# Kernel tuning notes

Hardware: AMD Instinct MI355X
Metric: run time of the kernel (lower is better)

## Reference

```python
import jax, jax.numpy as jnp
import numpy as np

N_NODES = 50000
N_EDGES = 400000
N_GRAPHS = 250
D = 256
NUM_FEATURES = 256
NUM_CLASSES = 10
N_EXTRA_LAYERS = 4  # num_layers - 1
BN_EPS = 1e-5


def _mean_agg(x, src, dst, n):
    # DGL copy_u + mean over incoming edges; zero in-degree nodes get 0.
    s = jax.ops.segment_sum(x[src], dst, num_segments=n)           # [N, d]
    deg = jax.ops.segment_sum(jnp.ones((src.shape[0],), x.dtype), dst, num_segments=n)
    deg = deg[:, None]
    return jnp.where(deg > 0, s / jnp.maximum(deg, 1.0), 0.0)


def _gin_layer(x, src, dst, W1, b1, W2, b2, gamma, beta):
    n = x.shape[0]
    h = x + _mean_agg(x, src, dst, n)                              # (1+eps)*x + agg, eps=0
    h = jax.nn.relu(h @ W1 + b1) @ W2 + b2                         # apply_func MLP
    h = jax.nn.relu(h)                                             # GINConv activation
    mu = h.mean(axis=0)
    var = h.var(axis=0)                                            # biased var (torch BN train)
    return gamma * (h - mu) / jnp.sqrt(var + BN_EPS) + beta


def setup_inputs() -> dict:
    key = jax.random.key(0)
    ks = jax.random.split(key, 24)
    sc_in = 1.0 / np.sqrt(NUM_FEATURES)
    sc = 1.0 / np.sqrt(D)
    inp = {
        "x": jax.random.normal(ks[0], (N_NODES, NUM_FEATURES), dtype=jnp.float32),
        "src": jax.random.randint(ks[1], (N_EDGES,), 0, N_NODES, dtype=jnp.int32),
        "dst": jax.random.randint(ks[2], (N_EDGES,), 0, N_NODES, dtype=jnp.int32),
        "node_counts": jnp.full((N_GRAPHS,), N_NODES // N_GRAPHS, dtype=jnp.int32),
        # conv1 MLP + BN1
        "W1a": jax.random.normal(ks[3], (NUM_FEATURES, D), dtype=jnp.float32) * sc_in,
        "b1a": jnp.zeros((D,), jnp.float32),
        "W1b": jax.random.normal(ks[4], (D, D), dtype=jnp.float32) * sc,
        "b1b": jnp.zeros((D,), jnp.float32),
        "g1": jnp.ones((D,), jnp.float32),
        "be1": jnp.zeros((D,), jnp.float32),
        # stacked convs 2..5 + BNs
        "Ws1": jax.random.normal(ks[5], (N_EXTRA_LAYERS, D, D), dtype=jnp.float32) * sc,
        "bs1": jnp.zeros((N_EXTRA_LAYERS, D), jnp.float32),
        "Ws2": jax.random.normal(ks[6], (N_EXTRA_LAYERS, D, D), dtype=jnp.float32) * sc,
        "bs2": jnp.zeros((N_EXTRA_LAYERS, D), jnp.float32),
        "gammas": jnp.ones((N_EXTRA_LAYERS, D), jnp.float32),
        "betas": jnp.zeros((N_EXTRA_LAYERS, D), jnp.float32),
        # classifier
        "fcW1": jax.random.normal(ks[7], (D, D), dtype=jnp.float32) * sc,
        "fcb1": jnp.zeros((D,), jnp.float32),
        "fcW2": jax.random.normal(ks[8], (D, NUM_CLASSES), dtype=jnp.float32) * sc,
        "fcb2": jnp.zeros((NUM_CLASSES,), jnp.float32),
    }
    return inp


def reference(x, src, dst, node_counts, W1a, b1a, W1b, b1b, g1, be1,
              Ws1, bs1, Ws2, bs2, gammas, betas, fcW1, fcb1, fcW2, fcb2):
    h = _gin_layer(x, src, dst, W1a, b1a, W1b, b1b, g1, be1)
    for i in range(N_EXTRA_LAYERS):
        h = _gin_layer(h, src, dst, Ws1[i], bs1[i], Ws2[i], bs2[i], gammas[i], betas[i])
    # per-graph last-node readout
    last_idx = jnp.cumsum(node_counts) - 1                          # [n_graphs]
    g = h[last_idx]                                                 # [n_graphs, d]
    # dropout is identity in eval mode
    g = jax.nn.relu(g @ fcW1 + fcb1)
    logits = g @ fcW2 + fcb2
    return jax.nn.log_softmax(logits, axis=-1)
```

## Files before the change

kernel.cpp:

```cpp
#include <hip/hip_runtime.h>
#include <hip/hip_bf16.h>

#define N_NODESC 50000
#define N_EDGESC 400000
#define N_GRAPHSC 250
#define DDIM 256
#define NCLS 10
#define BN_EPSF 1e-5f
#define MPAD 50048
#define NBLK_SCAN 196

typedef __attribute__((ext_vector_type(4))) float f32x4;
typedef __attribute__((ext_vector_type(8))) short bf16x8;
typedef __attribute__((ext_vector_type(8))) unsigned short u16x8;

__device__ __forceinline__ float bf2f(unsigned short h) {
    union { unsigned int u; float f; } c;
    c.u = ((unsigned int)h) << 16;
    return c.f;
}
__device__ __forceinline__ unsigned short f2bf(float f) {
    union { float f; unsigned int u; } c;
    c.f = f;
    unsigned int u = c.u;
    return (unsigned short)((u + 0x7FFFu + ((u >> 16) & 1u)) >> 16);
}


__global__ void k_zero32(int* __restrict__ p, int n) {
    int i = blockIdx.x * blockDim.x + threadIdx.x;
    if (i < n) p[i] = 0;
}

__global__ void k_count(const int* __restrict__ dst, int* __restrict__ cnt) {
    int e = blockIdx.x * blockDim.x + threadIdx.x;
    if (e < N_EDGESC) atomicAdd(&cnt[dst[e]], 1);
}

__global__ __launch_bounds__(256) void k_scan1(const int* __restrict__ deg,
                                               int* __restrict__ rowstart,
                                               int* __restrict__ bsum) {
    __shared__ int sh[256];
    int tid = threadIdx.x;
    int i = blockIdx.x * 256 + tid;
    int v = (i < N_NODESC) ? deg[i] : 0;
    sh[tid] = v;
    __syncthreads();
    for (int off = 1; off < 256; off <<= 1) {
        int t = (tid >= off) ? sh[tid - off] : 0;
        __syncthreads();
        sh[tid] += t;
        __syncthreads();
    }
    if (i < N_NODESC) rowstart[i] = sh[tid] - v;
    if (tid == 255) bsum[blockIdx.x] = sh[255];
}

__global__ __launch_bounds__(256) void k_scan2(int* __restrict__ rowstart,
                                               const int* __restrict__ bsum) {
    __shared__ int sh[256];
    int tid = threadIdx.x;
    sh[tid] = (tid < NBLK_SCAN) ? bsum[tid] : 0;
    __syncthreads();
    for (int off = 1; off < 256; off <<= 1) {
        int t = (tid >= off) ? sh[tid - off] : 0;
        __syncthreads();
        sh[tid] += t;
        __syncthreads();
    }
    int i = blockIdx.x * 256 + tid;
    if (blockIdx.x > 0 && i < N_NODESC) rowstart[i] += sh[blockIdx.x - 1];
    if (i == 0) rowstart[N_NODESC] = N_EDGESC;
}

__global__ void k_fill(const int* __restrict__ src, const int* __restrict__ dst,
                       const int* __restrict__ rowstart, int* __restrict__ cur,
                       int* __restrict__ esrc) {
    int e = blockIdx.x * blockDim.x + threadIdx.x;
    if (e < N_EDGESC) {
        int d = dst[e];
        int pos = rowstart[d] + atomicAdd(&cur[d], 1);
        esrc[pos] = src[e];
    }
}


__global__ __launch_bounds__(256) void k_wprep(const float* __restrict__ W1a,
                                               const float* __restrict__ W1b,
                                               const float* __restrict__ Ws1,
                                               const float* __restrict__ Ws2,
                                               unsigned short* __restrict__ Wt) {
    int i = blockIdx.x * blockDim.x + threadIdx.x;
    if (i >= 10 * 65536) return;
    int m = i >> 16;
    int r = i & 65535;
    int n = r >> 8;
    int k = r & 255;
    int l = m >> 1, wsel = m & 1;
    const float* src = (l == 0) ? (wsel ? W1b : W1a)
                                : (wsel ? Ws2 + (size_t)(l - 1) * 65536
                                        : Ws1 + (size_t)(l - 1) * 65536);
    Wt[i] = f2bf(src[(size_t)k * 256 + n]);
}

__global__ __launch_bounds__(256) void k_xbf(const float* __restrict__ X,
                                             unsigned short* __restrict__ Y) {
    int i = blockIdx.x * 256 + threadIdx.x;
    if (i < N_NODESC * 64) {
        float4 v = ((const float4*)X)[i];
        ushort4 o;
        o.x = f2bf(v.x); o.y = f2bf(v.y); o.z = f2bf(v.z); o.w = f2bf(v.w);
        ((ushort4*)Y)[i] = o;
    }
}

__global__ void k_zeropad(unsigned short* __restrict__ b1) {
    int i = blockIdx.x * blockDim.x + threadIdx.x;
    int npad = (MPAD - N_NODESC) * DDIM;
    if (i < npad) b1[(size_t)N_NODESC * DDIM + i] = 0;
}

__global__ __launch_bounds__(256) void k_agg_bf(const unsigned short* __restrict__ X,
                                                const int* __restrict__ esrc,
                                                const int* __restrict__ rowstart,
                                                const float* __restrict__ stat,
                                                const float* __restrict__ gamma,
                                                const float* __restrict__ beta,
                                                unsigned short* __restrict__ Hout) {
    int node = blockIdx.x * 4 + (threadIdx.x >> 6);
    if (node >= N_NODESC) return;
    int lane = threadIdx.x & 63;
    int d0 = lane * 4;
    float sc[4], tt[4];
    if (stat) {
        const float invN = 1.0f / (float)N_NODESC;
#pragma unroll
        for (int q = 0; q < 4; q++) {
            float mu = stat[d0 + q] * invN;
            float var = stat[256 + d0 + q] * invN - mu * mu;
            float s = gamma[d0 + q] * rsqrtf(var + BN_EPSF);
            sc[q] = s;
            tt[q] = beta[d0 + q] - s * mu;
        }
    } else {
#pragma unroll
        for (int q = 0; q < 4; q++) { sc[q] = 1.f; tt[q] = 0.f; }
    }
    int beg = rowstart[node];
    int end = rowstart[node + 1];
    float a0 = 0.f, a1 = 0.f, a2 = 0.f, a3 = 0.f;
    float b0 = 0.f, b1 = 0.f, b2 = 0.f, b3 = 0.f;
    float c0 = 0.f, c1 = 0.f, c2 = 0.f, c3 = 0.f;
    float e0 = 0.f, e1 = 0.f, e2 = 0.f, e3 = 0.f;
    int j = beg;
    for (; j + 4 <= end; j += 4) {
        int sn0 = esrc[j], sn1 = esrc[j + 1], sn2 = esrc[j + 2], sn3 = esrc[j + 3];
        ushort4 v0 = *(const ushort4*)(X + (size_t)sn0 * DDIM + d0);
        ushort4 v1 = *(const ushort4*)(X + (size_t)sn1 * DDIM + d0);
        ushort4 v2 = *(const ushort4*)(X + (size_t)sn2 * DDIM + d0);
        ushort4 v3 = *(const ushort4*)(X + (size_t)sn3 * DDIM + d0);
        a0 += bf2f(v0.x); a1 += bf2f(v0.y); a2 += bf2f(v0.z); a3 += bf2f(v0.w);
        b0 += bf2f(v1.x); b1 += bf2f(v1.y); b2 += bf2f(v1.z); b3 += bf2f(v1.w);
        c0 += bf2f(v2.x); c1 += bf2f(v2.y); c2 += bf2f(v2.z); c3 += bf2f(v2.w);
        e0 += bf2f(v3.x); e1 += bf2f(v3.y); e2 += bf2f(v3.z); e3 += bf2f(v3.w);
    }
    for (; j < end; j++) {
        int sn0 = esrc[j];
        ushort4 v0 = *(const ushort4*)(X + (size_t)sn0 * DDIM + d0);
        a0 += bf2f(v0.x); a1 += bf2f(v0.y); a2 += bf2f(v0.z); a3 += bf2f(v0.w);
    }
    a0 += b0 + c0 + e0; a1 += b1 + c1 + e1; a2 += b2 + c2 + e2; a3 += b3 + c3 + e3;
    float inv = (end > beg) ? 1.0f / (float)(end - beg) : 0.0f;
    float cnt = (end > beg) ? 2.0f : 1.0f;
    ushort4 xv = *(const ushort4*)(X + (size_t)node * DDIM + d0);
    ushort4 o;
    o.x = f2bf(sc[0] * (bf2f(xv.x) + a0 * inv) + tt[0] * cnt);
    o.y = f2bf(sc[1] * (bf2f(xv.y) + a1 * inv) + tt[1] * cnt);
    o.z = f2bf(sc[2] * (bf2f(xv.z) + a2 * inv) + tt[2] * cnt);
    o.w = f2bf(sc[3] * (bf2f(xv.w) + a3 * inv) + tt[3] * cnt);
    *(ushort4*)(Hout + (size_t)node * DDIM + d0) = o;
}


__global__ __launch_bounds__(512, 4) void k_mlp(const unsigned short* __restrict__ A,
                                                const unsigned short* __restrict__ W1t,
                                                const float* __restrict__ b1,
                                                const unsigned short* __restrict__ W2t,
                                                const float* __restrict__ b2,
                                                unsigned short* __restrict__ C,
                                                float* __restrict__ stat) {
    __shared__ unsigned short Tl[128 * 256];

    const int tid = threadIdx.x;
    const int wv = tid >> 6;
    const int lane = tid & 63;
    const int bm = blockIdx.x;
    const int wr = (wv >> 2) * 64;
    const int wc = (wv & 3) * 64;
    const int lr = lane & 15;
    const int lk = lane >> 4;

    f32x4 acc[4][4];

#pragma unroll
    for (int m = 0; m < 4; m++)
#pragma unroll
        for (int n = 0; n < 4; n++) acc[m][n] = (f32x4)(0.f);

    for (int k0 = 0; k0 < 256; k0 += 32) {
        bf16x8 af[4], bfr[4];
#pragma unroll
        for (int m = 0; m < 4; m++)
            af[m] = *(const bf16x8*)(A + (size_t)(bm * 128 + wr + m * 16 + lr) * 256 +
                                     k0 + lk * 8);
#pragma unroll
        for (int n = 0; n < 4; n++)
            bfr[n] = *(const bf16x8*)(W1t + (size_t)(wc + n * 16 + lr) * 256 +
                                      k0 + lk * 8);
#pragma unroll
        for (int m = 0; m < 4; m++)
#pragma unroll
            for (int n = 0; n < 4; n++)
                acc[m][n] = __builtin_amdgcn_mfma_f32_16x16x32_bf16(af[m], bfr[n],
                                                                    acc[m][n], 0, 0, 0);
    }
#pragma unroll
    for (int n = 0; n < 4; n++) {
        int col = wc + n * 16 + lr;
        float bv = b1[col];
#pragma unroll
        for (int m = 0; m < 4; m++)
#pragma unroll
            for (int i = 0; i < 4; i++) {
                int row = wr + m * 16 + lk * 4 + i;
                float v = fmaxf(acc[m][n][i] + bv, 0.f);
                int cs = (col >> 3) ^ (row & 7);
                Tl[row * 256 + cs * 8 + (col & 7)] = f2bf(v);
            }
    }
    __syncthreads();

#pragma unroll
    for (int m = 0; m < 4; m++)
#pragma unroll
        for (int n = 0; n < 4; n++) acc[m][n] = (f32x4)(0.f);

    for (int k0 = 0; k0 < 256; k0 += 32) {
        bf16x8 af[4], bfr[4];
#pragma unroll
        for (int m = 0; m < 4; m++) {
            int row = wr + m * 16 + lr;
            int cs = ((k0 >> 3) + lk) ^ (row & 7);
            af[m] = ((const bf16x8*)Tl)[row * 32 + cs];
        }
#pragma unroll
        for (int n = 0; n < 4; n++)
            bfr[n] = *(const bf16x8*)(W2t + (size_t)(wc + n * 16 + lr) * 256 +
                                      k0 + lk * 8);
#pragma unroll
        for (int m = 0; m < 4; m++)
#pragma unroll
            for (int n = 0; n < 4; n++)
                acc[m][n] = __builtin_amdgcn_mfma_f32_16x16x32_bf16(af[m], bfr[n],
                                                                    acc[m][n], 0, 0, 0);
    }
#pragma unroll
    for (int n = 0; n < 4; n++) {
        int col = wc + n * 16 + lr;
        float bv = b2[col];
        float sp = 0.f, ssp = 0.f;
#pragma unroll
        for (int m = 0; m < 4; m++)
#pragma unroll
            for (int i = 0; i < 4; i++) {
                int row = bm * 128 + wr + m * 16 + lk * 4 + i;
                float v = fmaxf(acc[m][n][i] + bv, 0.f);
                C[(size_t)row * 256 + col] = f2bf(v);
                if (row < N_NODESC) { sp += v; ssp += v * v; }
            }
        sp += __shfl_xor(sp, 16);
        sp += __shfl_xor(sp, 32);
        ssp += __shfl_xor(ssp, 16);
        ssp += __shfl_xor(ssp, 32);
        if (lane < 16) {
            atomicAdd(&stat[col], sp);
            atomicAdd(&stat[256 + col], ssp);
        }
    }
}


__global__ __launch_bounds__(256) void k_head(const unsigned short* __restrict__ Y,
                                              const int* __restrict__ counts,
                                              const float* __restrict__ stat,
                                              const float* __restrict__ gamma,
                                              const float* __restrict__ beta,
                                              const float* __restrict__ fcW1,
                                              const float* __restrict__ fcb1,
                                              const float* __restrict__ fcW2,
                                              const float* __restrict__ fcb2,
                                              float* __restrict__ out) {
    int g = blockIdx.x;
    __shared__ float row[DDIM];
    __shared__ float gv[DDIM];
    __shared__ float logits[NCLS];
    __shared__ int lastIdx;
    if (threadIdx.x == 0) {
        int s = 0;
        for (int i = 0; i <= g; i++) s += counts[i];
        lastIdx = s - 1;
    }
    __syncthreads();
    int j = threadIdx.x;
    const float invN = 1.0f / (float)N_NODESC;
    float mu = stat[j] * invN;
    float var = stat[256 + j] * invN - mu * mu;
    float sc = gamma[j] * rsqrtf(var + BN_EPSF);
    row[j] = sc * (bf2f(Y[(size_t)lastIdx * DDIM + j]) - mu) + beta[j];
    __syncthreads();
    float acc = fcb1[j];
    for (int d = 0; d < DDIM; d++) acc += row[d] * fcW1[(size_t)d * DDIM + j];
    gv[j] = fmaxf(acc, 0.f);
    __syncthreads();
    if (j < NCLS) {
        float a = fcb2[j];
        for (int d = 0; d < DDIM; d++) a += gv[d] * fcW2[(size_t)d * NCLS + j];
        logits[j] = a;
    }
    __syncthreads();
    if (j == 0) {
        float m = -1e30f;
        for (int c = 0; c < NCLS; c++) m = fmaxf(m, logits[c]);
        float se = 0.f;
        for (int c = 0; c < NCLS; c++) se += expf(logits[c] - m);
        float lse = m + logf(se);
        for (int c = 0; c < NCLS; c++) out[g * NCLS + c] = logits[c] - lse;
    }
}


extern "C" void kernel_launch(void* const* d_in, const int* in_sizes, int n_in,
                              void* d_out, int out_size, void* d_ws, size_t ws_size,
                              hipStream_t stream) {
    const float* x    = (const float*)d_in[0];
    const int* src    = (const int*)d_in[1];
    const int* dst    = (const int*)d_in[2];
    const int* counts = (const int*)d_in[3];
    const float* W1a  = (const float*)d_in[4];
    const float* b1a  = (const float*)d_in[5];
    const float* W1b  = (const float*)d_in[6];
    const float* b1b  = (const float*)d_in[7];
    const float* g1   = (const float*)d_in[8];
    const float* be1  = (const float*)d_in[9];
    const float* Ws1  = (const float*)d_in[10];
    const float* bs1  = (const float*)d_in[11];
    const float* Ws2  = (const float*)d_in[12];
    const float* bs2  = (const float*)d_in[13];
    const float* gms  = (const float*)d_in[14];
    const float* bts  = (const float*)d_in[15];
    const float* fcW1 = (const float*)d_in[16];
    const float* fcb1 = (const float*)d_in[17];
    const float* fcW2 = (const float*)d_in[18];
    const float* fcb2 = (const float*)d_in[19];
    float* out = (float*)d_out;

    char* ws = (char*)d_ws;
    const size_t BUF = (size_t)MPAD * DDIM * 2;
    unsigned short* B0 = (unsigned short*)(ws);
    unsigned short* B1 = (unsigned short*)(ws + BUF);
    unsigned short* Bx = (unsigned short*)(ws + 2 * BUF);
    unsigned short* Wt = (unsigned short*)(ws + 3 * BUF);
    int* rowstart      = (int*)(ws + 3 * BUF + 1310720);
    int* cursor        = (int*)(ws + 3 * BUF + 1510784);
    int* esrc          = (int*)(ws + 3 * BUF + 1710848);
    float* colsum      = (float*)(ws + 3 * BUF + 3310848);
    int* bsum          = (int*)(ws + 3 * BUF + 3312896);

    k_zero32<<<dim3((N_NODESC + 255) / 256), 256, 0, stream>>>(cursor, N_NODESC);
    k_count<<<dim3((N_EDGESC + 255) / 256), 256, 0, stream>>>(dst, cursor);
    k_scan1<<<dim3(NBLK_SCAN), 256, 0, stream>>>(cursor, rowstart, bsum);
    k_scan2<<<dim3(NBLK_SCAN), 256, 0, stream>>>(rowstart, bsum);
    k_zero32<<<dim3((N_NODESC + 255) / 256), 256, 0, stream>>>(cursor, N_NODESC);
    k_fill<<<dim3((N_EDGESC + 255) / 256), 256, 0, stream>>>(src, dst, rowstart,
                                                             cursor, esrc);

    k_wprep<<<dim3((10 * 65536 + 255) / 256), 256, 0, stream>>>(W1a, W1b, Ws1, Ws2, Wt);
    k_xbf<<<dim3(12500), 256, 0, stream>>>(x, Bx);
    k_zeropad<<<dim3(((MPAD - N_NODESC) * DDIM + 255) / 256), 256, 0, stream>>>(B1);

    for (int l = 0; l < 5; ++l) {
        const float* B1b = (l == 0) ? b1a : bs1 + (l - 1) * 256;
        const float* B2b = (l == 0) ? b1b : bs2 + (l - 1) * 256;
        const unsigned short* Wt1 = Wt + (size_t)(l * 2) * 65536;
        const unsigned short* Wt2 = Wt + (size_t)(l * 2 + 1) * 65536;

        if (l == 0) {
            k_agg_bf<<<dim3(12500), 256, 0, stream>>>(Bx, esrc, rowstart, nullptr,
                                                      nullptr, nullptr, B1);
        } else {
            const float* GA = (l == 1) ? g1 : gms + (l - 2) * 256;
            const float* BE = (l == 1) ? be1 : bts + (l - 2) * 256;
            k_agg_bf<<<dim3(12500), 256, 0, stream>>>(B0, esrc, rowstart, colsum,
                                                      GA, BE, B1);
        }
        k_zero32<<<1, 512, 0, stream>>>((int*)colsum, 512);
        k_mlp<<<dim3(MPAD / 128), 512, 0, stream>>>(B1, Wt1, B1b, Wt2, B2b, B0,
                                                    colsum);
    }

    k_head<<<dim3(N_GRAPHSC), 256, 0, stream>>>(B0, counts, colsum,
                                                gms + 3 * 256, bts + 3 * 256,
                                                fcW1, fcb1, fcW2, fcb2, out);
}
```

Baseline: 587.6 us.

## Fuse neighbor aggregation into the MLP kernel with LDS-staged tiles

Merges the per-layer aggregation kernel and the two-GEMM MLP kernel into one kernel. Each block gathers and normalizes 64 node rows straight into shared memory and then runs both matmuls on that tile. The output is staged back through shared memory so global stores are coalesced. Per-layer BN stats move into separate buffers that are zeroed once, which removes the per-layer zero kernels and the pad-zero kernel. This saves a full write and read of the aggregated activations plus launches, at the cost of a smaller 64-row tile with 4 waves that each cover all rows and 64 columns, and a gather phase that now runs inside the MFMA kernel.

```diff
diff --git a/kernel.cpp b/kernel.cpp
--- a/kernel.cpp
+++ b/kernel.cpp
@@ -114,92 +114,89 @@
     }
 }
 
-__global__ void k_zeropad(unsigned short* __restrict__ b1) {
-    int i = blockIdx.x * blockDim.x + threadIdx.x;
-    int npad = (MPAD - N_NODESC) * DDIM;
-    if (i < npad) b1[(size_t)N_NODESC * DDIM + i] = 0;
-}
-
-__global__ __launch_bounds__(256) void k_agg_bf(const unsigned short* __restrict__ X,
-                                                const int* __restrict__ esrc,
-                                                const int* __restrict__ rowstart,
-                                                const float* __restrict__ stat,
-                                                const float* __restrict__ gamma,
-                                                const float* __restrict__ beta,
-                                                unsigned short* __restrict__ Hout) {
-    int node = blockIdx.x * 4 + (threadIdx.x >> 6);
-    if (node >= N_NODESC) return;
-    int lane = threadIdx.x & 63;
-    int d0 = lane * 4;
-    float sc[4], tt[4];
-    if (stat) {
-        const float invN = 1.0f / (float)N_NODESC;
-#pragma unroll
-        for (int q = 0; q < 4; q++) {
-            float mu = stat[d0 + q] * invN;
-            float var = stat[256 + d0 + q] * invN - mu * mu;
-            float s = gamma[d0 + q] * rsqrtf(var + BN_EPSF);
-            sc[q] = s;
-            tt[q] = beta[d0 + q] - s * mu;
-        }
-    } else {
-#pragma unroll
-        for (int q = 0; q < 4; q++) { sc[q] = 1.f; tt[q] = 0.f; }
-    }
-    int beg = rowstart[node];
-    int end = rowstart[node + 1];
-    float a0 = 0.f, a1 = 0.f, a2 = 0.f, a3 = 0.f;
-    float b0 = 0.f, b1 = 0.f, b2 = 0.f, b3 = 0.f;
-    float c0 = 0.f, c1 = 0.f, c2 = 0.f, c3 = 0.f;
-    float e0 = 0.f, e1 = 0.f, e2 = 0.f, e3 = 0.f;
-    int j = beg;
-    for (; j + 4 <= end; j += 4) {
-        int sn0 = esrc[j], sn1 = esrc[j + 1], sn2 = esrc[j + 2], sn3 = esrc[j + 3];
-        ushort4 v0 = *(const ushort4*)(X + (size_t)sn0 * DDIM + d0);
-        ushort4 v1 = *(const ushort4*)(X + (size_t)sn1 * DDIM + d0);
-        ushort4 v2 = *(const ushort4*)(X + (size_t)sn2 * DDIM + d0);
-        ushort4 v3 = *(const ushort4*)(X + (size_t)sn3 * DDIM + d0);
-        a0 += bf2f(v0.x); a1 += bf2f(v0.y); a2 += bf2f(v0.z); a3 += bf2f(v0.w);
-        b0 += bf2f(v1.x); b1 += bf2f(v1.y); b2 += bf2f(v1.z); b3 += bf2f(v1.w);
-        c0 += bf2f(v2.x); c1 += bf2f(v2.y); c2 += bf2f(v2.z); c3 += bf2f(v2.w);
-        e0 += bf2f(v3.x); e1 += bf2f(v3.y); e2 += bf2f(v3.z); e3 += bf2f(v3.w);
-    }
-    for (; j < end; j++) {
-        int sn0 = esrc[j];
-        ushort4 v0 = *(const ushort4*)(X + (size_t)sn0 * DDIM + d0);
-        a0 += bf2f(v0.x); a1 += bf2f(v0.y); a2 += bf2f(v0.z); a3 += bf2f(v0.w);
-    }
-    a0 += b0 + c0 + e0; a1 += b1 + c1 + e1; a2 += b2 + c2 + e2; a3 += b3 + c3 + e3;
-    float inv = (end > beg) ? 1.0f / (float)(end - beg) : 0.0f;
-    float cnt = (end > beg) ? 2.0f : 1.0f;
-    ushort4 xv = *(const ushort4*)(X + (size_t)node * DDIM + d0);
-    ushort4 o;
-    o.x = f2bf(sc[0] * (bf2f(xv.x) + a0 * inv) + tt[0] * cnt);
-    o.y = f2bf(sc[1] * (bf2f(xv.y) + a1 * inv) + tt[1] * cnt);
-    o.z = f2bf(sc[2] * (bf2f(xv.z) + a2 * inv) + tt[2] * cnt);
-    o.w = f2bf(sc[3] * (bf2f(xv.w) + a3 * inv) + tt[3] * cnt);
-    *(ushort4*)(Hout + (size_t)node * DDIM + d0) = o;
-}
-
-
-__global__ __launch_bounds__(512, 4) void k_mlp(const unsigned short* __restrict__ A,
-                                                const unsigned short* __restrict__ W1t,
-                                                const float* __restrict__ b1,
-                                                const unsigned short* __restrict__ W2t,
-                                                const float* __restrict__ b2,
-                                                unsigned short* __restrict__ C,
-                                                float* __restrict__ stat) {
-    __shared__ unsigned short Tl[128 * 256];
+
+__global__ __launch_bounds__(256, 2) void k_layer(
+    const unsigned short* __restrict__ X, const int* __restrict__ esrc,
+    const int* __restrict__ rowstart, const float* __restrict__ stat_in,
+    const float* __restrict__ gamma_in, const float* __restrict__ beta_in,
+    const unsigned short* __restrict__ W1t, const float* __restrict__ b1,
+    const unsigned short* __restrict__ W2t, const float* __restrict__ b2,
+    unsigned short* __restrict__ C, float* __restrict__ stat_out) {
+    __shared__ unsigned short At[64 * 256];
+    __shared__ unsigned short Tl[64 * 256];
+    __shared__ float scl[256];
+    __shared__ float ttl[256];
 
     const int tid = threadIdx.x;
     const int wv = tid >> 6;
     const int lane = tid & 63;
+    const int half = lane >> 5;
+    const int cg = lane & 31;
     const int bm = blockIdx.x;
-    const int wr = (wv >> 2) * 64;
-    const int wc = (wv & 3) * 64;
+
+    if (stat_in) {
+        const float invN = 1.0f / (float)N_NODESC;
+        float mu = stat_in[tid] * invN;
+        float var = stat_in[256 + tid] * invN - mu * mu;
+        float s = gamma_in[tid] * rsqrtf(var + BN_EPSF);
+        scl[tid] = s;
+        ttl[tid] = beta_in[tid] - s * mu;
+    } else {
+        scl[tid] = 1.f;
+        ttl[tid] = 0.f;
+    }
+    __syncthreads();
+
+    {
+        const int d0 = cg * 8;
+        for (int slot = 0; slot < 8; slot++) {
+            int r = wv * 16 + slot * 2 + half;
+            int node = bm * 64 + r;
+            float s0[8], s1[8];
+#pragma unroll
+            for (int q = 0; q < 8; q++) { s0[q] = 0.f; s1[q] = 0.f; }
+            int deg = 0;
+            u16x8 o;
+            if (node < N_NODESC) {
+                int beg = rowstart[node];
+                int end = rowstart[node + 1];
+                deg = end - beg;
+                int e = beg;
+                for (; e + 1 < end; e += 2) {
+                    int sn0 = esrc[e], sn1 = esrc[e + 1];
+                    u16x8 v0 = *(const u16x8*)(X + (size_t)sn0 * DDIM + d0);
+                    u16x8 v1 = *(const u16x8*)(X + (size_t)sn1 * DDIM + d0);
+#pragma unroll
+                    for (int q = 0; q < 8; q++) {
+                        s0[q] += bf2f(v0[q]);
+                        s1[q] += bf2f(v1[q]);
+                    }
+                }
+                if (e < end) {
+                    int sn0 = esrc[e];
+                    u16x8 v0 = *(const u16x8*)(X + (size_t)sn0 * DDIM + d0);
+#pragma unroll
+                    for (int q = 0; q < 8; q++) s0[q] += bf2f(v0[q]);
+                }
+                float inv = (deg > 0) ? 1.0f / (float)deg : 0.0f;
+                float cnt = (deg > 0) ? 2.0f : 1.0f;
+                u16x8 xv = *(const u16x8*)(X + (size_t)node * DDIM + d0);
+#pragma unroll
+                for (int q = 0; q < 8; q++)
+                    o[q] = f2bf(scl[d0 + q] * (bf2f(xv[q]) + (s0[q] + s1[q]) * inv) +
+                                ttl[d0 + q] * cnt);
+            } else {
+#pragma unroll
+                for (int q = 0; q < 8; q++) o[q] = 0;
+            }
+            *(u16x8*)&At[r * 256 + (cg ^ (r & 7)) * 8] = o;
+        }
+    }
+    __syncthreads();
+
+    const int wc = wv * 64;
     const int lr = lane & 15;
     const int lk = lane >> 4;
-
     f32x4 acc[4][4];
 
 #pragma unroll
@@ -210,9 +207,10 @@
     for (int k0 = 0; k0 < 256; k0 += 32) {
         bf16x8 af[4], bfr[4];
 #pragma unroll
-        for (int m = 0; m < 4; m++)
-            af[m] = *(const bf16x8*)(A + (size_t)(bm * 128 + wr + m * 16 + lr) * 256 +
-                                     k0 + lk * 8);
+        for (int m = 0; m < 4; m++) {
+            int row = m * 16 + lr;
+            af[m] = ((const bf16x8*)At)[row * 32 + (((k0 >> 3) + lk) ^ (row & 7))];
+        }
 #pragma unroll
         for (int n = 0; n < 4; n++)
             bfr[n] = *(const bf16x8*)(W1t + (size_t)(wc + n * 16 + lr) * 256 +
@@ -232,10 +230,9 @@
         for (int m = 0; m < 4; m++)
 #pragma unroll
             for (int i = 0; i < 4; i++) {
-                int row = wr + m * 16 + lk * 4 + i;
+                int row = m * 16 + lk * 4 + i;
                 float v = fmaxf(acc[m][n][i] + bv, 0.f);
-                int cs = (col >> 3) ^ (row & 7);
-                Tl[row * 256 + cs * 8 + (col & 7)] = f2bf(v);
+                Tl[row * 256 + ((col >> 3) ^ (row & 7)) * 8 + (col & 7)] = f2bf(v);
             }
     }
     __syncthreads();
@@ -249,9 +246,8 @@
         bf16x8 af[4], bfr[4];
 #pragma unroll
         for (int m = 0; m < 4; m++) {
-            int row = wr + m * 16 + lr;
-            int cs = ((k0 >> 3) + lk) ^ (row & 7);
-            af[m] = ((const bf16x8*)Tl)[row * 32 + cs];
+            int row = m * 16 + lr;
+            af[m] = ((const bf16x8*)Tl)[row * 32 + (((k0 >> 3) + lk) ^ (row & 7))];
         }
 #pragma unroll
         for (int n = 0; n < 4; n++)
@@ -273,19 +269,29 @@
         for (int m = 0; m < 4; m++)
 #pragma unroll
             for (int i = 0; i < 4; i++) {
-                int row = bm * 128 + wr + m * 16 + lk * 4 + i;
+                int row = m * 16 + lk * 4 + i;
                 float v = fmaxf(acc[m][n][i] + bv, 0.f);
-                C[(size_t)row * 256 + col] = f2bf(v);
-                if (row < N_NODESC) { sp += v; ssp += v * v; }
+                At[row * 256 + ((col >> 3) ^ (row & 7)) * 8 + (col & 7)] = f2bf(v);
+                if (bm * 64 + row < N_NODESC) { sp += v; ssp += v * v; }
             }
         sp += __shfl_xor(sp, 16);
         sp += __shfl_xor(sp, 32);
         ssp += __shfl_xor(ssp, 16);
         ssp += __shfl_xor(ssp, 32);
         if (lane < 16) {
-            atomicAdd(&stat[col], sp);
-            atomicAdd(&stat[256 + col], ssp);
+            atomicAdd(&stat_out[col], sp);
+            atomicAdd(&stat_out[256 + col], ssp);
         }
+    }
+    __syncthreads();
+
+#pragma unroll
+    for (int it = 0; it < 8; it++) {
+        int chunk = it * 256 + tid;
+        int row = chunk >> 5;
+        int cc = chunk & 31;
+        u16x8 v = *(const u16x8*)&At[row * 256 + (cc ^ (row & 7)) * 8];
+        *(u16x8*)(C + (size_t)(bm * 64 + row) * DDIM + cc * 8) = v;
     }
 }
 
@@ -373,8 +379,8 @@
     int* rowstart      = (int*)(ws + 3 * BUF + 1310720);
     int* cursor        = (int*)(ws + 3 * BUF + 1510784);
     int* esrc          = (int*)(ws + 3 * BUF + 1710848);
-    float* colsum      = (float*)(ws + 3 * BUF + 3310848);
-    int* bsum          = (int*)(ws + 3 * BUF + 3312896);
+    float* stats       = (float*)(ws + 3 * BUF + 3310848);
+    int* bsum          = (int*)(ws + 3 * BUF + 3321088);
 
     k_zero32<<<dim3((N_NODESC + 255) / 256), 256, 0, stream>>>(cursor, N_NODESC);
     k_count<<<dim3((N_EDGESC + 255) / 256), 256, 0, stream>>>(dst, cursor);
@@ -386,29 +392,25 @@
 
     k_wprep<<<dim3((10 * 65536 + 255) / 256), 256, 0, stream>>>(W1a, W1b, Ws1, Ws2, Wt);
     k_xbf<<<dim3(12500), 256, 0, stream>>>(x, Bx);
-    k_zeropad<<<dim3(((MPAD - N_NODESC) * DDIM + 255) / 256), 256, 0, stream>>>(B1);
+    k_zero32<<<dim3(10), 256, 0, stream>>>((int*)stats, 2560);
 
     for (int l = 0; l < 5; ++l) {
+        const unsigned short* IN = (l == 0) ? Bx : ((l & 1) ? B0 : B1);
+        unsigned short* OUT = (l & 1) ? B1 : B0;
         const float* B1b = (l == 0) ? b1a : bs1 + (l - 1) * 256;
         const float* B2b = (l == 0) ? b1b : bs2 + (l - 1) * 256;
         const unsigned short* Wt1 = Wt + (size_t)(l * 2) * 65536;
         const unsigned short* Wt2 = Wt + (size_t)(l * 2 + 1) * 65536;
-
-        if (l == 0) {
-            k_agg_bf<<<dim3(12500), 256, 0, stream>>>(Bx, esrc, rowstart, nullptr,
-                                                      nullptr, nullptr, B1);
-        } else {
-            const float* GA = (l == 1) ? g1 : gms + (l - 2) * 256;
-            const float* BE = (l == 1) ? be1 : bts + (l - 2) * 256;
-            k_agg_bf<<<dim3(12500), 256, 0, stream>>>(B0, esrc, rowstart, colsum,
-                                                      GA, BE, B1);
-        }
-        k_zero32<<<1, 512, 0, stream>>>((int*)colsum, 512);
-        k_mlp<<<dim3(MPAD / 128), 512, 0, stream>>>(B1, Wt1, B1b, Wt2, B2b, B0,
-                                                    colsum);
-    }
-
-    k_head<<<dim3(N_GRAPHSC), 256, 0, stream>>>(B0, counts, colsum,
+        const float* stat_in = (l == 0) ? nullptr : stats + (size_t)(l - 1) * 512;
+        const float* GA = (l == 0) ? nullptr : ((l == 1) ? g1 : gms + (l - 2) * 256);
+        const float* BE = (l == 0) ? nullptr : ((l == 1) ? be1 : bts + (l - 2) * 256);
+
+        k_layer<<<dim3(MPAD / 64), 256, 0, stream>>>(
+            IN, esrc, rowstart, stat_in, GA, BE, Wt1, B1b, Wt2, B2b, OUT,
+            stats + (size_t)l * 512);
+    }
+
+    k_head<<<dim3(N_GRAPHSC), 256, 0, stream>>>(B0, counts, stats + 4 * 512,
                                                 gms + 3 * 256, bts + 3 * 256,
                                                 fcW1, fcb1, fcW2, fcb2, out);
 }
```

New measurement: 672.7 us. 1.14x slower.

## Prefetch MLP weight fragments and stage output through LDS for coalesced stores

Applied to the files above, without the earlier changes.

In k_mlp the B-operand weight fragments for the next k-step are now loaded one step ahead (register double-buffering) in both GEMMs. The second GEMM's result is written into the swizzled LDS tile and then copied out as coalesced 16-byte row stores, replacing the scattered 2-byte global stores. The per-layer colsum zeroing launches are replaced by one upfront zero of a per-layer stats array, and the pad zeroing kernel is dropped. The min-occupancy hint is removed from launch bounds, which may change register allocation and occupancy; the prefetch adds registers and the LDS staging adds extra syncs.

```diff
diff --git a/kernel.cpp b/kernel.cpp
--- a/kernel.cpp
+++ b/kernel.cpp
@@ -112,12 +112,6 @@
         o.x = f2bf(v.x); o.y = f2bf(v.y); o.z = f2bf(v.z); o.w = f2bf(v.w);
         ((ushort4*)Y)[i] = o;
     }
-}
-
-__global__ void k_zeropad(unsigned short* __restrict__ b1) {
-    int i = blockIdx.x * blockDim.x + threadIdx.x;
-    int npad = (MPAD - N_NODESC) * DDIM;
-    if (i < npad) b1[(size_t)N_NODESC * DDIM + i] = 0;
 }
 
 __global__ __launch_bounds__(256) void k_agg_bf(const unsigned short* __restrict__ X,
@@ -182,13 +176,13 @@
 }
 
 
-__global__ __launch_bounds__(512, 4) void k_mlp(const unsigned short* __restrict__ A,
-                                                const unsigned short* __restrict__ W1t,
-                                                const float* __restrict__ b1,
-                                                const unsigned short* __restrict__ W2t,
-                                                const float* __restrict__ b2,
-                                                unsigned short* __restrict__ C,
-                                                float* __restrict__ stat) {
+__global__ __launch_bounds__(512) void k_mlp(const unsigned short* __restrict__ A,
+                                             const unsigned short* __restrict__ W1t,
+                                             const float* __restrict__ b1,
+                                             const unsigned short* __restrict__ W2t,
+                                             const float* __restrict__ b2,
+                                             unsigned short* __restrict__ C,
+                                             float* __restrict__ stat) {
     __shared__ unsigned short Tl[128 * 256];
 
     const int tid = threadIdx.x;
@@ -201,28 +195,37 @@
     const int lk = lane >> 4;
 
     f32x4 acc[4][4];
+    bf16x8 bcur[4], bnxt[4];
 
 #pragma unroll
     for (int m = 0; m < 4; m++)
 #pragma unroll
         for (int n = 0; n < 4; n++) acc[m][n] = (f32x4)(0.f);
 
+#pragma unroll
+    for (int n = 0; n < 4; n++)
+        bcur[n] = *(const bf16x8*)(W1t + (size_t)(wc + n * 16 + lr) * 256 + lk * 8);
+
     for (int k0 = 0; k0 < 256; k0 += 32) {
-        bf16x8 af[4], bfr[4];
+        bf16x8 af[4];
 #pragma unroll
         for (int m = 0; m < 4; m++)
             af[m] = *(const bf16x8*)(A + (size_t)(bm * 128 + wr + m * 16 + lr) * 256 +
                                      k0 + lk * 8);
-#pragma unroll
-        for (int n = 0; n < 4; n++)
-            bfr[n] = *(const bf16x8*)(W1t + (size_t)(wc + n * 16 + lr) * 256 +
-                                      k0 + lk * 8);
+        if (k0 < 224) {
+#pragma unroll
+            for (int n = 0; n < 4; n++)
+                bnxt[n] = *(const bf16x8*)(W1t + (size_t)(wc + n * 16 + lr) * 256 +
+                                           k0 + 32 + lk * 8);
+        }
 #pragma unroll
         for (int m = 0; m < 4; m++)
 #pragma unroll
             for (int n = 0; n < 4; n++)
-                acc[m][n] = __builtin_amdgcn_mfma_f32_16x16x32_bf16(af[m], bfr[n],
+                acc[m][n] = __builtin_amdgcn_mfma_f32_16x16x32_bf16(af[m], bcur[n],
                                                                     acc[m][n], 0, 0, 0);
+#pragma unroll
+        for (int n = 0; n < 4; n++) bcur[n] = bnxt[n];
     }
 #pragma unroll
     for (int n = 0; n < 4; n++) {
@@ -234,8 +237,7 @@
             for (int i = 0; i < 4; i++) {
                 int row = wr + m * 16 + lk * 4 + i;
                 float v = fmaxf(acc[m][n][i] + bv, 0.f);
-                int cs = (col >> 3) ^ (row & 7);
-                Tl[row * 256 + cs * 8 + (col & 7)] = f2bf(v);
+                Tl[row * 256 + ((col >> 3) ^ (row & 7)) * 8 + (col & 7)] = f2bf(v);
             }
     }
     __syncthreads();
@@ -245,25 +247,34 @@
 #pragma unroll
         for (int n = 0; n < 4; n++) acc[m][n] = (f32x4)(0.f);
 
+#pragma unroll
+    for (int n = 0; n < 4; n++)
+        bcur[n] = *(const bf16x8*)(W2t + (size_t)(wc + n * 16 + lr) * 256 + lk * 8);
+
     for (int k0 = 0; k0 < 256; k0 += 32) {
-        bf16x8 af[4], bfr[4];
+        bf16x8 af[4];
 #pragma unroll
         for (int m = 0; m < 4; m++) {
             int row = wr + m * 16 + lr;
-            int cs = ((k0 >> 3) + lk) ^ (row & 7);
-            af[m] = ((const bf16x8*)Tl)[row * 32 + cs];
-        }
-#pragma unroll
-        for (int n = 0; n < 4; n++)
-            bfr[n] = *(const bf16x8*)(W2t + (size_t)(wc + n * 16 + lr) * 256 +
-                                      k0 + lk * 8);
+            af[m] = ((const bf16x8*)Tl)[row * 32 + (((k0 >> 3) + lk) ^ (row & 7))];
+        }
+        if (k0 < 224) {
+#pragma unroll
+            for (int n = 0; n < 4; n++)
+                bnxt[n] = *(const bf16x8*)(W2t + (size_t)(wc + n * 16 + lr) * 256 +
+                                           k0 + 32 + lk * 8);
+        }
 #pragma unroll
         for (int m = 0; m < 4; m++)
 #pragma unroll
             for (int n = 0; n < 4; n++)
-                acc[m][n] = __builtin_amdgcn_mfma_f32_16x16x32_bf16(af[m], bfr[n],
+                acc[m][n] = __builtin_amdgcn_mfma_f32_16x16x32_bf16(af[m], bcur[n],
                                                                     acc[m][n], 0, 0, 0);
-    }
+#pragma unroll
+        for (int n = 0; n < 4; n++) bcur[n] = bnxt[n];
+    }
+    __syncthreads();
+
 #pragma unroll
     for (int n = 0; n < 4; n++) {
         int col = wc + n * 16 + lr;
@@ -273,10 +284,10 @@
         for (int m = 0; m < 4; m++)
 #pragma unroll
             for (int i = 0; i < 4; i++) {
-                int row = bm * 128 + wr + m * 16 + lk * 4 + i;
+                int row = wr + m * 16 + lk * 4 + i;
                 float v = fmaxf(acc[m][n][i] + bv, 0.f);
-                C[(size_t)row * 256 + col] = f2bf(v);
-                if (row < N_NODESC) { sp += v; ssp += v * v; }
+                Tl[row * 256 + ((col >> 3) ^ (row & 7)) * 8 + (col & 7)] = f2bf(v);
+                if (bm * 128 + row < N_NODESC) { sp += v; ssp += v * v; }
             }
         sp += __shfl_xor(sp, 16);
         sp += __shfl_xor(sp, 32);
@@ -286,6 +297,16 @@
             atomicAdd(&stat[col], sp);
             atomicAdd(&stat[256 + col], ssp);
         }
+    }
+    __syncthreads();
+
+#pragma unroll
+    for (int it = 0; it < 8; it++) {
+        int chunk = it * 512 + tid;
+        int row = chunk >> 5;
+        int cc = chunk & 31;
+        u16x8 v = *(const u16x8*)&Tl[row * 256 + (cc ^ (row & 7)) * 8];
+        *(u16x8*)(C + (size_t)(bm * 128 + row) * DDIM + cc * 8) = v;
     }
 }
 
@@ -373,8 +394,8 @@
     int* rowstart      = (int*)(ws + 3 * BUF + 1310720);
     int* cursor        = (int*)(ws + 3 * BUF + 1510784);
     int* esrc          = (int*)(ws + 3 * BUF + 1710848);
-    float* colsum      = (float*)(ws + 3 * BUF + 3310848);
-    int* bsum          = (int*)(ws + 3 * BUF + 3312896);
+    float* stats       = (float*)(ws + 3 * BUF + 3310848);
+    int* bsum          = (int*)(ws + 3 * BUF + 3321088);
 
     k_zero32<<<dim3((N_NODESC + 255) / 256), 256, 0, stream>>>(cursor, N_NODESC);
     k_count<<<dim3((N_EDGESC + 255) / 256), 256, 0, stream>>>(dst, cursor);
@@ -386,7 +407,7 @@
 
     k_wprep<<<dim3((10 * 65536 + 255) / 256), 256, 0, stream>>>(W1a, W1b, Ws1, Ws2, Wt);
     k_xbf<<<dim3(12500), 256, 0, stream>>>(x, Bx);
-    k_zeropad<<<dim3(((MPAD - N_NODESC) * DDIM + 255) / 256), 256, 0, stream>>>(B1);
+    k_zero32<<<dim3(10), 256, 0, stream>>>((int*)stats, 2560);
 
     for (int l = 0; l < 5; ++l) {
         const float* B1b = (l == 0) ? b1a : bs1 + (l - 1) * 256;
@@ -400,15 +421,15 @@
         } else {
             const float* GA = (l == 1) ? g1 : gms + (l - 2) * 256;
             const float* BE = (l == 1) ? be1 : bts + (l - 2) * 256;
-            k_agg_bf<<<dim3(12500), 256, 0, stream>>>(B0, esrc, rowstart, colsum,
+            k_agg_bf<<<dim3(12500), 256, 0, stream>>>(B0, esrc, rowstart,
+                                                      stats + (size_t)(l - 1) * 512,
                                                       GA, BE, B1);
         }
-        k_zero32<<<1, 512, 0, stream>>>((int*)colsum, 512);
         k_mlp<<<dim3(MPAD / 128), 512, 0, stream>>>(B1, Wt1, B1b, Wt2, B2b, B0,
-                                                    colsum);
-    }
-
-    k_head<<<dim3(N_GRAPHSC), 256, 0, stream>>>(B0, counts, colsum,
+                                                    stats + (size_t)l * 512);
+    }
+
+    k_head<<<dim3(N_GRAPHSC), 256, 0, stream>>>(B0, counts, stats + 4 * 512,
                                                 gms + 3 * 256, bts + 3 * 256,
                                                 fcW1, fcb1, fcW2, fcb2, out);
 }
```

Result: slower. 636.4 us (+8.3%).

## Split fused MLP into two LDS-staged GEMMs with deterministic BN stat reduction

Applied to the files above, without the earlier changes.

The fused two-layer MLP kernel is replaced by a generic 128x128-tile GEMM launched twice per layer, with the intermediate activation going through a new global buffer. The GEMM stages A and W tiles into swizzled LDS using global_load_lds, and writes output through an LDS tile so the global stores are coalesced. BatchNorm column statistics move from global atomics to per-block partial sums plus a two-stage reduction, and per-layer stats buffers replace the zeroing launch. This adds an extra global round trip of the intermediate activations and more kernel launches. The padding-zeroing kernel is also removed.

```diff
diff --git a/kernel.cpp b/kernel.cpp
--- a/kernel.cpp
+++ b/kernel.cpp
@@ -8,6 +8,7 @@
 #define NCLS 10
 #define BN_EPSF 1e-5f
 #define MPAD 50048
+#define NBLK_GEMM 391
 #define NBLK_SCAN 196
 
 typedef __attribute__((ext_vector_type(4))) float f32x4;
@@ -24,6 +25,12 @@
     c.f = f;
     unsigned int u = c.u;
     return (unsigned short)((u + 0x7FFFu + ((u >> 16) & 1u)) >> 16);
+}
+
+__device__ __forceinline__ void gld_lds16(const void* g, void* l) {
+    __builtin_amdgcn_global_load_lds(
+        (const __attribute__((address_space(1))) unsigned int*)g,
+        (__attribute__((address_space(3))) unsigned int*)l, 16, 0, 0);
 }
 
 
@@ -114,11 +121,6 @@
     }
 }
 
-__global__ void k_zeropad(unsigned short* __restrict__ b1) {
-    int i = blockIdx.x * blockDim.x + threadIdx.x;
-    int npad = (MPAD - N_NODESC) * DDIM;
-    if (i < npad) b1[(size_t)N_NODESC * DDIM + i] = 0;
-}
 
 __global__ __launch_bounds__(256) void k_agg_bf(const unsigned short* __restrict__ X,
                                                 const int* __restrict__ esrc,
@@ -182,111 +184,127 @@
 }
 
 
-__global__ __launch_bounds__(512, 4) void k_mlp(const unsigned short* __restrict__ A,
-                                                const unsigned short* __restrict__ W1t,
-                                                const float* __restrict__ b1,
-                                                const unsigned short* __restrict__ W2t,
-                                                const float* __restrict__ b2,
-                                                unsigned short* __restrict__ C,
-                                                float* __restrict__ stat) {
-    __shared__ unsigned short Tl[128 * 256];
+__global__ __launch_bounds__(256) void k_gemm(const unsigned short* __restrict__ A,
+                                              const unsigned short* __restrict__ Wt,
+                                              const float* __restrict__ bias,
+                                              unsigned short* __restrict__ C,
+                                              float* __restrict__ part) {
+    __shared__ unsigned short As[128 * 32];
+    __shared__ unsigned short Bs[128 * 32];
+    __shared__ unsigned short Ct[128 * 128];
+    __shared__ float sred[2][256];
 
     const int tid = threadIdx.x;
     const int wv = tid >> 6;
     const int lane = tid & 63;
     const int bm = blockIdx.x;
-    const int wr = (wv >> 2) * 64;
-    const int wc = (wv & 3) * 64;
+    const int bn = blockIdx.y;
+
+    const int wr = (wv >> 1) * 64;
+    const int wc = (wv & 1) * 64;
     const int lr = lane & 15;
     const int lk = lane >> 4;
 
     f32x4 acc[4][4];
-
 #pragma unroll
     for (int m = 0; m < 4; m++)
 #pragma unroll
         for (int n = 0; n < 4; n++) acc[m][n] = (f32x4)(0.f);
 
     for (int k0 = 0; k0 < 256; k0 += 32) {
+#pragma unroll
+        for (int i = 0; i < 2; i++) {
+            int c = wv * 128 + i * 64 + lane;
+            int row = c >> 2;
+            int kc = (c & 3) ^ ((row >> 1) & 3);
+            const unsigned short* ga = A + (size_t)(bm * 128 + row) * 256 + k0 + kc * 8;
+            gld_lds16(ga, (void*)&As[(size_t)(wv * 128 + i * 64) * 8]);
+            const unsigned short* gb = Wt + (size_t)(bn * 128 + row) * 256 + k0 + kc * 8;
+            gld_lds16(gb, (void*)&Bs[(size_t)(wv * 128 + i * 64) * 8]);
+        }
+        __syncthreads();
+
         bf16x8 af[4], bfr[4];
 #pragma unroll
-        for (int m = 0; m < 4; m++)
-            af[m] = *(const bf16x8*)(A + (size_t)(bm * 128 + wr + m * 16 + lr) * 256 +
-                                     k0 + lk * 8);
-#pragma unroll
-        for (int n = 0; n < 4; n++)
-            bfr[n] = *(const bf16x8*)(W1t + (size_t)(wc + n * 16 + lr) * 256 +
-                                      k0 + lk * 8);
+        for (int m = 0; m < 4; m++) {
+            int row = wr + m * 16 + lr;
+            af[m] = ((const bf16x8*)As)[row * 4 + (lk ^ ((row >> 1) & 3))];
+        }
+#pragma unroll
+        for (int n = 0; n < 4; n++) {
+            int row = wc + n * 16 + lr;
+            bfr[n] = ((const bf16x8*)Bs)[row * 4 + (lk ^ ((row >> 1) & 3))];
+        }
 #pragma unroll
         for (int m = 0; m < 4; m++)
 #pragma unroll
             for (int n = 0; n < 4; n++)
                 acc[m][n] = __builtin_amdgcn_mfma_f32_16x16x32_bf16(af[m], bfr[n],
                                                                     acc[m][n], 0, 0, 0);
-    }
+        __syncthreads();
+    }
+
 #pragma unroll
     for (int n = 0; n < 4; n++) {
-        int col = wc + n * 16 + lr;
-        float bv = b1[col];
+        int cloc = wc + n * 16 + lr;
+        float bv = bias[bn * 128 + cloc];
+        float sp = 0.f, ssp = 0.f;
 #pragma unroll
         for (int m = 0; m < 4; m++)
 #pragma unroll
             for (int i = 0; i < 4; i++) {
                 int row = wr + m * 16 + lk * 4 + i;
                 float v = fmaxf(acc[m][n][i] + bv, 0.f);
-                int cs = (col >> 3) ^ (row & 7);
-                Tl[row * 256 + cs * 8 + (col & 7)] = f2bf(v);
+                Ct[row * 128 + (((cloc >> 3) ^ (row & 7)) << 3) + (cloc & 7)] = f2bf(v);
+                if (bm * 128 + row < N_NODESC) { sp += v; ssp += v * v; }
             }
-    }
-    __syncthreads();
-
-#pragma unroll
-    for (int m = 0; m < 4; m++)
-#pragma unroll
-        for (int n = 0; n < 4; n++) acc[m][n] = (f32x4)(0.f);
-
-    for (int k0 = 0; k0 < 256; k0 += 32) {
-        bf16x8 af[4], bfr[4];
-#pragma unroll
-        for (int m = 0; m < 4; m++) {
-            int row = wr + m * 16 + lr;
-            int cs = ((k0 >> 3) + lk) ^ (row & 7);
-            af[m] = ((const bf16x8*)Tl)[row * 32 + cs];
-        }
-#pragma unroll
-        for (int n = 0; n < 4; n++)
-            bfr[n] = *(const bf16x8*)(W2t + (size_t)(wc + n * 16 + lr) * 256 +
-                                      k0 + lk * 8);
-#pragma unroll
-        for (int m = 0; m < 4; m++)
-#pragma unroll
-            for (int n = 0; n < 4; n++)
-                acc[m][n] = __builtin_amdgcn_mfma_f32_16x16x32_bf16(af[m], bfr[n],
-                                                                    acc[m][n], 0, 0, 0);
-    }
-#pragma unroll
-    for (int n = 0; n < 4; n++) {
-        int col = wc + n * 16 + lr;
-        float bv = b2[col];
-        float sp = 0.f, ssp = 0.f;
-#pragma unroll
-        for (int m = 0; m < 4; m++)
-#pragma unroll
-            for (int i = 0; i < 4; i++) {
-                int row = bm * 128 + wr + m * 16 + lk * 4 + i;
-                float v = fmaxf(acc[m][n][i] + bv, 0.f);
-                C[(size_t)row * 256 + col] = f2bf(v);
-                if (row < N_NODESC) { sp += v; ssp += v * v; }
+        if (part) {
+            sp += __shfl_xor(sp, 16);
+            sp += __shfl_xor(sp, 32);
+            ssp += __shfl_xor(ssp, 16);
+            ssp += __shfl_xor(ssp, 32);
+            if (lane < 16) {
+                sred[wv >> 1][cloc] = sp;
+                sred[wv >> 1][128 + cloc] = ssp;
             }
-        sp += __shfl_xor(sp, 16);
-        sp += __shfl_xor(sp, 32);
-        ssp += __shfl_xor(ssp, 16);
-        ssp += __shfl_xor(ssp, 32);
-        if (lane < 16) {
-            atomicAdd(&stat[col], sp);
-            atomicAdd(&stat[256 + col], ssp);
-        }
-    }
+        }
+    }
+    __syncthreads();
+
+#pragma unroll
+    for (int it = 0; it < 8; it++) {
+        int chunk = it * 256 + tid;
+        int row = chunk >> 4;
+        int cc = chunk & 15;
+        u16x8 v = *(const u16x8*)&Ct[row * 128 + ((cc ^ (row & 7)) << 3)];
+        *(u16x8*)(C + (size_t)(bm * 128 + row) * DDIM + bn * 128 + cc * 8) = v;
+    }
+    if (part && tid < 256) {
+        float v = sred[0][tid] + sred[1][tid];
+        int cloc = tid & 127;
+        int off = (tid < 128) ? (bn * 128 + cloc) : (256 + bn * 128 + cloc);
+        part[(size_t)bm * 512 + off] = v;
+    }
+}
+
+
+__global__ __launch_bounds__(512) void k_statred1(const float* __restrict__ part,
+                                                  float* __restrict__ part2) {
+    int t = threadIdx.x;
+    int b0 = blockIdx.x * 17;
+    float s = 0.f;
+#pragma unroll 4
+    for (int j = 0; j < 17; j++) s += part[(size_t)(b0 + j) * 512 + t];
+    part2[(size_t)blockIdx.x * 512 + t] = s;
+}
+
+__global__ __launch_bounds__(512) void k_statred2(const float* __restrict__ part2,
+                                                  float* __restrict__ stat) {
+    int t = threadIdx.x;
+    float s = 0.f;
+#pragma unroll 4
+    for (int j = 0; j < 23; j++) s += part2[(size_t)j * 512 + t];
+    stat[t] = s;
 }
 
 
@@ -368,13 +386,16 @@
     const size_t BUF = (size_t)MPAD * DDIM * 2;
     unsigned short* B0 = (unsigned short*)(ws);
     unsigned short* B1 = (unsigned short*)(ws + BUF);
-    unsigned short* Bx = (unsigned short*)(ws + 2 * BUF);
-    unsigned short* Wt = (unsigned short*)(ws + 3 * BUF);
-    int* rowstart      = (int*)(ws + 3 * BUF + 1310720);
-    int* cursor        = (int*)(ws + 3 * BUF + 1510784);
-    int* esrc          = (int*)(ws + 3 * BUF + 1710848);
-    float* colsum      = (float*)(ws + 3 * BUF + 3310848);
-    int* bsum          = (int*)(ws + 3 * BUF + 3312896);
+    unsigned short* B2 = (unsigned short*)(ws + 2 * BUF);
+    unsigned short* Bx = (unsigned short*)(ws + 3 * BUF);
+    unsigned short* Wt = (unsigned short*)(ws + 4 * BUF);
+    int* rowstart      = (int*)(ws + 4 * BUF + 1310720);
+    int* cursor        = (int*)(ws + 4 * BUF + 1510784);
+    int* esrc          = (int*)(ws + 4 * BUF + 1710848);
+    float* stats       = (float*)(ws + 4 * BUF + 3310848);
+    int* bsum          = (int*)(ws + 4 * BUF + 3321088);
+    float* stats_part  = (float*)(ws + 4 * BUF + 3321872 + 16);
+    float* stats_part2 = (float*)(ws + 4 * BUF + 4122656 + 32);
 
     k_zero32<<<dim3((N_NODESC + 255) / 256), 256, 0, stream>>>(cursor, N_NODESC);
     k_count<<<dim3((N_EDGESC + 255) / 256), 256, 0, stream>>>(dst, cursor);
@@ -386,7 +407,6 @@
 
     k_wprep<<<dim3((10 * 65536 + 255) / 256), 256, 0, stream>>>(W1a, W1b, Ws1, Ws2, Wt);
     k_xbf<<<dim3(12500), 256, 0, stream>>>(x, Bx);
-    k_zeropad<<<dim3(((MPAD - N_NODESC) * DDIM + 255) / 256), 256, 0, stream>>>(B1);
 
     for (int l = 0; l < 5; ++l) {
         const float* B1b = (l == 0) ? b1a : bs1 + (l - 1) * 256;
@@ -400,15 +420,18 @@
         } else {
             const float* GA = (l == 1) ? g1 : gms + (l - 2) * 256;
             const float* BE = (l == 1) ? be1 : bts + (l - 2) * 256;
-            k_agg_bf<<<dim3(12500), 256, 0, stream>>>(B0, esrc, rowstart, colsum,
+            k_agg_bf<<<dim3(12500), 256, 0, stream>>>(B0, esrc, rowstart,
+                                                      stats + (size_t)(l - 1) * 512,
                                                       GA, BE, B1);
         }
-        k_zero32<<<1, 512, 0, stream>>>((int*)colsum, 512);
-        k_mlp<<<dim3(MPAD / 128), 512, 0, stream>>>(B1, Wt1, B1b, Wt2, B2b, B0,
-                                                    colsum);
-    }
-
-    k_head<<<dim3(N_GRAPHSC), 256, 0, stream>>>(B0, counts, colsum,
+        k_gemm<<<dim3(NBLK_GEMM, 2), 256, 0, stream>>>(B1, Wt1, B1b, B2, nullptr);
+        k_gemm<<<dim3(NBLK_GEMM, 2), 256, 0, stream>>>(B2, Wt2, B2b, B0, stats_part);
+        k_statred1<<<dim3(23), 512, 0, stream>>>(stats_part, stats_part2);
+        k_statred2<<<dim3(1), 512, 0, stream>>>(stats_part2,
+                                                stats + (size_t)l * 512);
+    }
+
+    k_head<<<dim3(N_GRAPHSC), 256, 0, stream>>>(B0, counts, stats + 4 * 512,
                                                 gms + 3 * 256, bts + 3 * 256,
                                                 fcW1, fcb1, fcW2, fcb2, out);
 }
```

Result: faster. 540.6 us (-8.0%).
